# Kernel optimization log

Measured on AMD Instinct MI355X. Metric: run time of the kernel, lower is better.

## Reference

```python
import jax, jax.numpy as jnp
import numpy as np

R = 3            # window radius -> (2R+1)^2 = 49 neighbors
N = 128          # grid side, n
K = 131          # 3 + 64 + 64 channels
C = 21           # num_classes
B = 2            # batch
W = (2 * R + 1) ** 2


def setup_inputs() -> dict:
    key = jax.random.key(0)
    k1, k2, k3, k4 = jax.random.split(key, 4)
    return {
        "intergrated": jax.random.normal(k1, (B, K, N, N), jnp.float32),
        "x2": jax.random.normal(k2, (B, C, N * N), jnp.float32),
        "sel_mask": jax.random.randint(k3, (B, N, N), 0, 2).astype(jnp.int32),
        "conv_parameter": jax.random.uniform(k4, (K,), jnp.float32),
    }


def _shifts(x, r):
    """Gather (2r+1)^2 shifted copies: x [..., n, n] -> [..., n, n, W].
    Entry w=(di,dj) holds x[i+di-r, j+dj-r] (zero-padded out of bounds)."""
    n = x.shape[-1]
    pad = [(0, 0)] * (x.ndim - 2) + [(r, r), (r, r)]
    xp = jnp.pad(x, pad)
    cols = [xp[..., di:di + n, dj:dj + n]
            for di in range(2 * r + 1) for dj in range(2 * r + 1)]
    return jnp.stack(cols, axis=-1)


def _rwn_single(feats, x2b, maskb, conv_parameter):
    """feats [K,n,n], x2b [C,n^2], maskb [n,n] int -> y [n^2, C]."""
    n = feats.shape[-1]
    m = maskb.astype(feats.dtype)            # sampled-pixel indicator
    xm = feats * m                            # sparse-sampled features [K,n,n]
    nbr = _shifts(xm, R)                      # [K,n,n,W] neighbor values
    valid = _shifts(jnp.ones((n, n), feats.dtype), R) > 0  # [n,n,W] in-bounds
    # per-channel windowed L1 distance, exp, per-pixel normalization (softmax
    # of +distance over the valid window, as in the original code)
    d = jnp.abs(xm[..., None] - nbr)          # [K,n,n,W]
    e = jnp.where(valid[None], jnp.exp(d), 0.0)
    a = e / e.sum(axis=-1, keepdims=True)     # rows sum to 1 per channel
    # W = sum_k conv_parameter[k] * a_k, rows only for selected pixels
    A = jnp.einsum('k,kijw->ijw', conv_parameter, a) * m[..., None]  # [n,n,W]
    # y[q,c] = sum_p W[p,q] * x2[p,c]  (W^T @ x2^T, per original col/row swap)
    feat = x2b.reshape(C, n, n)
    msg = A[None] * feat[..., None]           # [C,n,n,W]
    ypad = jnp.zeros((C, n + 2 * R, n + 2 * R), feats.dtype)
    w = 0
    for di in range(2 * R + 1):
        for dj in range(2 * R + 1):
            ypad = ypad.at[:, di:di + n, dj:dj + n].add(msg[..., w])
            w += 1
    y = ypad[:, R:R + n, R:R + n].reshape(C, n * n)
    return y.T                                 # [n^2, C]


def reference(intergrated, x2, sel_mask, conv_parameter):
    f = lambda fe, xb, mb: _rwn_single(fe, xb, mb, conv_parameter)
    return jax.vmap(f)(intergrated, x2, sel_mask)  # [B, n^2, C]
```

## Files before the change

### kernel.cpp

```cpp
#include <hip/hip_runtime.h>
#include <hip/hip_fp16.h>

#define R_ 3
#define D_ 7
#define W_ 49
#define N_ 128
#define K_ 131
#define C_ 21
#define B_ 2
#define NN (N_ * N_)
#define TI_ 8
#define TJ_ 16
#define PROWS (TI_ + 2 * R_)
#define PCOLS (TJ_ + 2 * R_)
#define PSTR 24
#define NELEM (PROWS * PCOLS)
#define LDSP (PROWS * PSTR + 8)
#define KC 8
#define KCHUNK ((K_ + KC - 1) / KC)
#define HCELLS (PROWS * PCOLS)
#define NSLOT 28

typedef __fp16 h2 __attribute__((ext_vector_type(2)));

static __device__ __forceinline__ unsigned h2u(h2 x) { return __builtin_bit_cast(unsigned, x); }
static __device__ __forceinline__ h2 u2h(unsigned x) { return __builtin_bit_cast(h2, x); }

#if defined(__has_builtin)
#if __has_builtin(__builtin_amdgcn_fdot2)
#define FDOT2(a, b, c) __builtin_amdgcn_fdot2((a), (b), (c), false)
#endif
#endif
#ifndef FDOT2
#define FDOT2(a, b, c) ((c) + (float)(a)[0] * (float)(b)[0] + (float)(a)[1] * (float)(b)[1])
#endif

__global__ __launch_bounds__(256) void rwn_affinity_s(
    const float* __restrict__ feats,
    const int*   __restrict__ mask,
    const float* __restrict__ cp,
    unsigned* __restrict__ Asl)
{
    __shared__ unsigned patchw[LDSP];

    const int tile = blockIdx.x;
    const int kc   = blockIdx.y;
    const int b    = blockIdx.z;
    const int tr = tile >> 3, tc = tile & 7;
    const int ti0 = tr * TI_, tj0 = tc * TJ_;

    const int tid = threadIdx.x;
    const int pix = tid >> 1;
    const int h   = tid & 1;
    const int ti = pix >> 4;
    const int tj = pix & 15;
    const int gi = ti0 + ti, gj = tj0 + tj;

    const float LOG2E = 1.4426950408889634f;
    int   soff[2];
    float swt[2];
    float ozw[2];
    int   slds[2];
    #pragma unroll
    for (int r = 0; r < 2; ++r) {
        int e = tid + r * 256;
        bool act = (e < NELEM);
        int pr = e / PCOLS, pc = e - pr * PCOLS;
        int mi = ti0 + pr - R_, mj = tj0 + pc - R_;
        bool inb = act && mi >= 0 && mi < N_ && mj >= 0 && mj < N_;
        int cmi = mi < 0 ? 0 : (mi > N_ - 1 ? N_ - 1 : mi);
        int cmj = mj < 0 ? 0 : (mj > N_ - 1 ? N_ - 1 : mj);
        soff[r] = cmi * N_ + cmj;
        swt[r]  = inb ? ((float)mask[b * NN + soff[r]] * LOG2E) : 0.f;
        ozw[r]  = inb ? 1.f : 0.f;
        slds[r] = act ? (pr * PSTR + pc) : (PROWS * PSTR + 4);
    }

    const h2 ph2 = h ? (h2){(__fp16)1.f, (__fp16)0.f}
                     : (h2){(__fp16)1.f, (__fp16)1.f};
    const h2 one2 = (h2){(__fp16)1.f, (__fp16)1.f};
    const int cbase = (ti + R_) * PSTR + (tj + R_);
    const int bh = ti * PSTR + tj + 4 * h;

    h2 Aacc[14];
    #pragma unroll
    for (int i = 0; i < 14; ++i) Aacc[i] = (h2){(__fp16)0.f, (__fp16)0.f};

    const int k0 = kc * KCHUNK;
    const int k1 = (k0 + KCHUNK < K_) ? (k0 + KCHUNK) : K_;
    const float* fb = feats + (size_t)b * K_ * NN;

    for (int e = tid; e < LDSP; e += 256) patchw[e] = 0u;

    const float* fk0 = fb + (size_t)k0 * NN;
    float pre0 = fk0[soff[0]] * swt[0];
    float pre1 = fk0[soff[1]] * swt[1];

    __syncthreads();

    for (int k = k0; k < k1; ++k) {
        patchw[slds[0]] = h2u(__builtin_amdgcn_cvt_pkrtz(ozw[0] * exp2f(pre0),
                                                         ozw[0] * exp2f(-pre0)));
        patchw[slds[1]] = h2u(__builtin_amdgcn_cvt_pkrtz(ozw[1] * exp2f(pre1),
                                                         ozw[1] * exp2f(-pre1)));
        float n0 = 0.f, n1 = 0.f;
        if (k + 1 < k1) {
            const float* fn = fb + (size_t)(k + 1) * NN;
            n0 = fn[soff[0]] * swt[0];
            n1 = fn[soff[1]] * swt[1];
        }
        __syncthreads();

        const unsigned cw = patchw[cbase];
        const h2 cE2 = u2h(__builtin_amdgcn_perm(cw, cw, 0x01000100u));
        const h2 cI2 = u2h(__builtin_amdgcn_perm(cw, cw, 0x03020302u));

        h2 ex[14];
        float dsum = 0.f;
        #pragma unroll
        for (int u = 0; u < D_; ++u) {
            const int rb = bh + u * PSTR;
            const unsigned w0 = patchw[rb];
            const unsigned w1 = patchw[rb + 1];
            const unsigned w2 = patchw[rb + 2];
            const unsigned w3 = patchw[rb + 3];
            const h2 E01 = u2h(__builtin_amdgcn_perm(w1, w0, 0x05040100u));
            const h2 I01 = u2h(__builtin_amdgcn_perm(w1, w0, 0x07060302u));
            const h2 E23 = u2h(__builtin_amdgcn_perm(w3, w2, 0x05040100u));
            const h2 I23 = u2h(__builtin_amdgcn_perm(w3, w2, 0x07060302u));
            h2 t01 = __builtin_elementwise_max(cE2 * I01, E01 * cI2);
            h2 t23 = __builtin_elementwise_max(cE2 * I23, E23 * cI2);
            t23 = t23 * ph2;
            dsum = FDOT2(t01, one2, dsum);
            dsum = FDOT2(t23, one2, dsum);
            ex[u * 2]     = t01;
            ex[u * 2 + 1] = t23;
        }
        const float denom = dsum + __shfl_xor(dsum, 1, 64);
        const float scale = cp[k] * __frcp_rn(denom);
        const h2 s2 = __builtin_amdgcn_cvt_pkrtz(scale, scale);
        #pragma unroll
        for (int m = 0; m < 14; ++m) Aacc[m] = ex[m] * s2 + Aacc[m];
        __syncthreads();

        pre0 = n0; pre1 = n1;
    }

    const int mk = mask[b * NN + gi * N_ + gj];
    const h2 z2 = (h2){(__fp16)0.f, (__fp16)0.f};
    const int pixg = gi * N_ + gj;
    unsigned* ab = Asl + ((size_t)(kc * B_ + b) * NSLOT) * NN + pixg;
    #pragma unroll
    for (int u = 0; u < D_; ++u) {
        #pragma unroll
        for (int m = 0; m < 2; ++m) {
            const h2 tv = mk ? Aacc[u * 2 + m] : z2;
            ab[(size_t)(u * 4 + 2 * h + m) * NN] = h2u(tv);
        }
    }
}

__global__ __launch_bounds__(512) void rwn_gather_s(
    const unsigned* __restrict__ Asl,
    const float* __restrict__ x2,
    float* __restrict__ out)
{
    __shared__ float x2h[C_ * HCELLS];

    const int tile = blockIdx.x;
    const int b    = blockIdx.y;
    const int tr = tile >> 3, tc = tile & 7;
    const int gi0 = tr * TI_, gj0 = tc * TJ_;

    const int tid = threadIdx.x;

    const float* xb = x2 + (size_t)b * C_ * NN;
    for (int e = tid; e < C_ * HCELLS; e += 512) {
        const int c = e / HCELLS, cell = e - c * HCELLS;
        const int pr = cell / PCOLS, pc = cell - pr * PCOLS;
        const int mi = gi0 + pr - R_, mj = gj0 + pc - R_;
        const bool inb = (mi >= 0 && mi < N_ && mj >= 0 && mj < N_);
        const int cmi = mi < 0 ? 0 : (mi > N_ - 1 ? N_ - 1 : mi);
        const int cmj = mj < 0 ? 0 : (mj > N_ - 1 ? N_ - 1 : mj);
        x2h[e] = inb ? xb[c * NN + cmi * N_ + cmj] : 0.f;
    }
    __syncthreads();

    const int h = tid & 3;
    const int q = tid >> 2;
    const int qi = q >> 4, qj = q & 15;
    const int gi = gi0 + qi, gj = gj0 + qj;

    float av[13];
    int   cells[13];
    #pragma unroll
    for (int idx = 0; idx < 13; ++idx) {
        int w = h + 4 * idx;
        const float valid0 = (w < W_) ? 1.f : 0.f;
        if (w >= W_) w = 0;
        const int u = w / D_, vv = w - u * D_;
        const int s = vv >> 1, ln = vv & 1;
        const int pi = gi + R_ - u, pj = gj + R_ - vv;
        const int cmi = pi < 0 ? 0 : (pi > N_ - 1 ? N_ - 1 : pi);
        const int cmj = pj < 0 ? 0 : (pj > N_ - 1 ? N_ - 1 : pj);
        const float valid = (pi >= 0 && pi < N_ && pj >= 0 && pj < N_)
                          ? valid0 : 0.f;
        const int p = cmi * N_ + cmj;
        const size_t wordoff = (size_t)(u * 4 + s) * NN + p;
        float alo = 0.f, ahi = 0.f;
        #pragma unroll
        for (int kc = 0; kc < KC; ++kc) {
            const h2 pr2 = u2h(Asl[((size_t)(kc * B_ + b) * NSLOT) * NN + wordoff]);
            alo += (float)pr2[0];
            ahi += (float)pr2[1];
        }
        av[idx]    = valid * (ln ? ahi : alo);
        cells[idx] = (qi + 2 * R_ - u) * PCOLS + (qj + 2 * R_ - vv);
    }

    float acc[C_];
    #pragma unroll
    for (int c = 0; c < C_; ++c) acc[c] = 0.f;
    #pragma unroll
    for (int idx = 0; idx < 13; ++idx) {
        const float a = av[idx];
        const float* xc = x2h + cells[idx];
        #pragma unroll
        for (int c = 0; c < C_; ++c)
            acc[c] += a * xc[c * HCELLS];
    }

    #pragma unroll
    for (int c = 0; c < C_; ++c) {
        acc[c] += __shfl_xor(acc[c], 1, 64);
        acc[c] += __shfl_xor(acc[c], 2, 64);
    }

    __syncthreads();
    if (h == 0) {
        float* os = x2h + q * C_;
        #pragma unroll
        for (int c = 0; c < C_; ++c) os[c] = acc[c];
    }
    __syncthreads();
    for (int e = tid; e < TI_ * TJ_ * C_; e += 512) {
        const int qq = e / C_, cc = e - qq * C_;
        const int gq = (gi0 + (qq >> 4)) * N_ + gj0 + (qq & 15);
        out[((size_t)b * NN + gq) * C_ + cc] = x2h[e];
    }
}

__global__ __launch_bounds__(256) void rwn_affinity_at(
    const float* __restrict__ feats, const int* __restrict__ mask,
    const float* __restrict__ cp, float* __restrict__ Aout)
{
    __shared__ unsigned patchw[LDSP];
    const int tile = blockIdx.x, kc = blockIdx.y, b = blockIdx.z;
    const int tr = tile >> 3, tc = tile & 7;
    const int ti0 = tr * TI_, tj0 = tc * TJ_;
    const int tid = threadIdx.x;
    const int pix = tid >> 1, h = tid & 1;
    const int ti = pix >> 4, tj = pix & 15;
    const int gi = ti0 + ti, gj = tj0 + tj;
    const float LOG2E = 1.4426950408889634f;
    int soff[2]; float swt[2]; float ozw[2]; int slds[2];
    #pragma unroll
    for (int r = 0; r < 2; ++r) {
        int e = tid + r * 256;
        bool act = (e < NELEM);
        int pr = e / PCOLS, pc = e - pr * PCOLS;
        int mi = ti0 + pr - R_, mj = tj0 + pc - R_;
        bool inb = act && mi >= 0 && mi < N_ && mj >= 0 && mj < N_;
        int cmi = mi < 0 ? 0 : (mi > N_ - 1 ? N_ - 1 : mi);
        int cmj = mj < 0 ? 0 : (mj > N_ - 1 ? N_ - 1 : mj);
        soff[r] = cmi * N_ + cmj;
        swt[r]  = inb ? ((float)mask[b * NN + soff[r]] * LOG2E) : 0.f;
        ozw[r]  = inb ? 1.f : 0.f;
        slds[r] = act ? (pr * PSTR + pc) : (PROWS * PSTR + 4);
    }
    const h2 ph2 = h ? (h2){(__fp16)1.f, (__fp16)0.f}
                     : (h2){(__fp16)1.f, (__fp16)1.f};
    const h2 one2 = (h2){(__fp16)1.f, (__fp16)1.f};
    const int cbase = (ti + R_) * PSTR + (tj + R_);
    const int bh = ti * PSTR + tj + 4 * h;
    h2 Aacc[14];
    #pragma unroll
    for (int i = 0; i < 14; ++i) Aacc[i] = (h2){(__fp16)0.f, (__fp16)0.f};
    const int k0 = kc * KCHUNK;
    const int k1 = (k0 + KCHUNK < K_) ? (k0 + KCHUNK) : K_;
    const float* fb = feats + (size_t)b * K_ * NN;
    for (int e = tid; e < LDSP; e += 256) patchw[e] = 0u;
    const float* fk0 = fb + (size_t)k0 * NN;
    float pre0 = fk0[soff[0]] * swt[0];
    float pre1 = fk0[soff[1]] * swt[1];
    __syncthreads();
    for (int k = k0; k < k1; ++k) {
        patchw[slds[0]] = h2u(__builtin_amdgcn_cvt_pkrtz(ozw[0] * exp2f(pre0),
                                                         ozw[0] * exp2f(-pre0)));
        patchw[slds[1]] = h2u(__builtin_amdgcn_cvt_pkrtz(ozw[1] * exp2f(pre1),
                                                         ozw[1] * exp2f(-pre1)));
        float n0 = 0.f, n1 = 0.f;
        if (k + 1 < k1) {
            const float* fn = fb + (size_t)(k + 1) * NN;
            n0 = fn[soff[0]] * swt[0];
            n1 = fn[soff[1]] * swt[1];
        }
        __syncthreads();
        const unsigned cw = patchw[cbase];
        const h2 cE2 = u2h(__builtin_amdgcn_perm(cw, cw, 0x01000100u));
        const h2 cI2 = u2h(__builtin_amdgcn_perm(cw, cw, 0x03020302u));
        h2 ex[14];
        float dsum = 0.f;
        #pragma unroll
        for (int u = 0; u < D_; ++u) {
            const int rb = bh + u * PSTR;
            const unsigned w0 = patchw[rb];
            const unsigned w1 = patchw[rb + 1];
            const unsigned w2 = patchw[rb + 2];
            const unsigned w3 = patchw[rb + 3];
            const h2 E01 = u2h(__builtin_amdgcn_perm(w1, w0, 0x05040100u));
            const h2 I01 = u2h(__builtin_amdgcn_perm(w1, w0, 0x07060302u));
            const h2 E23 = u2h(__builtin_amdgcn_perm(w3, w2, 0x05040100u));
            const h2 I23 = u2h(__builtin_amdgcn_perm(w3, w2, 0x07060302u));
            h2 t01 = __builtin_elementwise_max(cE2 * I01, E01 * cI2);
            h2 t23 = __builtin_elementwise_max(cE2 * I23, E23 * cI2);
            t23 = t23 * ph2;
            dsum = FDOT2(t01, one2, dsum);
            dsum = FDOT2(t23, one2, dsum);
            ex[u * 2]     = t01;
            ex[u * 2 + 1] = t23;
        }
        const float denom = dsum + __shfl_xor(dsum, 1, 64);
        const float scale = cp[k] * __frcp_rn(denom);
        const h2 s2 = __builtin_amdgcn_cvt_pkrtz(scale, scale);
        #pragma unroll
        for (int m = 0; m < 14; ++m) Aacc[m] = ex[m] * s2 + Aacc[m];
        __syncthreads();
        pre0 = n0; pre1 = n1;
    }
    if (mask[b * NN + gi * N_ + gj] != 0) {
        const int pixg = gi * N_ + gj;
        float* ab = Aout + (size_t)b * W_ * NN + pixg;
        #pragma unroll
        for (int u = 0; u < D_; ++u) {
            #pragma unroll
            for (int m = 0; m < 2; ++m) {
                const h2 tv = Aacc[u * 2 + m];
                const int wbase = u * D_ + 4 * h + 2 * m;
                atomicAdd(ab + (size_t)wbase * NN, (float)tv[0]);
                if (h == 0 || m < 1)
                    atomicAdd(ab + (size_t)(wbase + 1) * NN, (float)tv[1]);
            }
        }
    }
}

__global__ __launch_bounds__(512) void rwn_gather_at(
    const float* __restrict__ Aarr, const float* __restrict__ x2,
    float* __restrict__ out)
{
    __shared__ float x2h[C_ * HCELLS];
    const int tile = blockIdx.x, b = blockIdx.y;
    const int tr = tile >> 3, tc = tile & 7;
    const int gi0 = tr * TI_, gj0 = tc * TJ_;
    const int tid = threadIdx.x;
    const float* xb = x2 + (size_t)b * C_ * NN;
    for (int e = tid; e < C_ * HCELLS; e += 512) {
        const int c = e / HCELLS, cell = e - c * HCELLS;
        const int pr = cell / PCOLS, pc = cell - pr * PCOLS;
        const int mi = gi0 + pr - R_, mj = gj0 + pc - R_;
        const bool inb = (mi >= 0 && mi < N_ && mj >= 0 && mj < N_);
        const int cmi = mi < 0 ? 0 : (mi > N_ - 1 ? N_ - 1 : mi);
        const int cmj = mj < 0 ? 0 : (mj > N_ - 1 ? N_ - 1 : mj);
        x2h[e] = inb ? xb[c * NN + cmi * N_ + cmj] : 0.f;
    }
    __syncthreads();
    const int h = tid & 3;
    const int q = tid >> 2;
    const int qi = q >> 4, qj = q & 15;
    const int gi = gi0 + qi, gj = gj0 + qj;
    const float* Ab = Aarr + (size_t)b * W_ * NN;
    float av[13];
    int   cells[13];
    #pragma unroll
    for (int idx = 0; idx < 13; ++idx) {
        int w = h + 4 * idx;
        const float valid = (w < W_) ? 1.f : 0.f;
        if (w >= W_) w = W_ - 1;
        const int u = w / D_, v = w - u * D_;
        const int pi = gi + R_ - u, pj = gj + R_ - v;
        const int cmi = pi < 0 ? 0 : (pi > N_ - 1 ? N_ - 1 : pi);
        const int cmj = pj < 0 ? 0 : (pj > N_ - 1 ? N_ - 1 : pj);
        av[idx]    = valid * Ab[(size_t)w * NN + cmi * N_ + cmj];
        cells[idx] = (qi + 2 * R_ - u) * PCOLS + (qj + 2 * R_ - v);
    }
    float acc[C_];
    #pragma unroll
    for (int c = 0; c < C_; ++c) acc[c] = 0.f;
    #pragma unroll
    for (int idx = 0; idx < 13; ++idx) {
        const float a = av[idx];
        const float* xc = x2h + cells[idx];
        #pragma unroll
        for (int c = 0; c < C_; ++c)
            acc[c] += a * xc[c * HCELLS];
    }
    #pragma unroll
    for (int c = 0; c < C_; ++c) {
        acc[c] += __shfl_xor(acc[c], 1, 64);
        acc[c] += __shfl_xor(acc[c], 2, 64);
    }
    __syncthreads();
    if (h == 0) {
        float* os = x2h + q * C_;
        #pragma unroll
        for (int c = 0; c < C_; ++c) os[c] = acc[c];
    }
    __syncthreads();
    for (int e = tid; e < TI_ * TJ_ * C_; e += 512) {
        const int qq = e / C_, cc = e - qq * C_;
        const int gq = (gi0 + (qq >> 4)) * N_ + gj0 + (qq & 15);
        out[((size_t)b * NN + gq) * C_ + cc] = x2h[e];
    }
}

extern "C" void kernel_launch(void* const* d_in, const int* in_sizes, int n_in,
                              void* d_out, int out_size, void* d_ws, size_t ws_size,
                              hipStream_t stream) {
    const float* feats = (const float*)d_in[0];
    const float* x2    = (const float*)d_in[1];
    const int*   mask  = (const int*)d_in[2];
    const float* cp    = (const float*)d_in[3];
    float* out = (float*)d_out;

    const size_t need = (size_t)KC * B_ * NSLOT * NN * sizeof(unsigned);

    if (ws_size >= need) {
        unsigned* Asl = (unsigned*)d_ws;
        dim3 gridA(128, KC, B_);
        rwn_affinity_s<<<gridA, 256, 0, stream>>>(feats, mask, cp, Asl);
        dim3 gridG(128, B_);
        rwn_gather_s<<<gridG, 512, 0, stream>>>(Asl, x2, out);
    } else {
        float* Aarr = (float*)d_ws;
        const size_t Abytes = (size_t)B_ * W_ * NN * sizeof(float);
        (void)hipMemsetAsync(Aarr, 0, Abytes, stream);
        dim3 gridA(128, KC, B_);
        rwn_affinity_at<<<gridA, 256, 0, stream>>>(feats, mask, cp, Aarr);
        dim3 gridG(128, B_);
        rwn_gather_at<<<gridG, 512, 0, stream>>>(Aarr, x2, out);
    }
}
```

Before: 138.3 us.

## Process two channels per iteration with packed half2 lanes in affinity kernel

```diff
diff --git a/kernel.cpp b/kernel.cpp
--- a/kernel.cpp
+++ b/kernel.cpp
@@ -16,24 +16,16 @@
 #define PSTR 24
 #define NELEM (PROWS * PCOLS)
 #define LDSP (PROWS * PSTR + 8)
-#define KC 8
-#define KCHUNK ((K_ + KC - 1) / KC)
+#define KC 6
+#define KCHUNK 22
 #define HCELLS (PROWS * PCOLS)
 #define NSLOT 28
 
 typedef __fp16 h2 __attribute__((ext_vector_type(2)));
+typedef __fp16 h4 __attribute__((ext_vector_type(4)));
 
 static __device__ __forceinline__ unsigned h2u(h2 x) { return __builtin_bit_cast(unsigned, x); }
 static __device__ __forceinline__ h2 u2h(unsigned x) { return __builtin_bit_cast(h2, x); }
-
-#if defined(__has_builtin)
-#if __has_builtin(__builtin_amdgcn_fdot2)
-#define FDOT2(a, b, c) __builtin_amdgcn_fdot2((a), (b), (c), false)
-#endif
-#endif
-#ifndef FDOT2
-#define FDOT2(a, b, c) ((c) + (float)(a)[0] * (float)(b)[0] + (float)(a)[1] * (float)(b)[1])
-#endif
 
 __global__ __launch_bounds__(256) void rwn_affinity_s(
     const float* __restrict__ feats,
@@ -41,7 +33,7 @@
     const float* __restrict__ cp,
     unsigned* __restrict__ Asl)
 {
-    __shared__ unsigned patchw[LDSP];
+    __shared__ h4 patch4[LDSP];
 
     const int tile = blockIdx.x;
     const int kc   = blockIdx.y;
@@ -76,86 +68,124 @@
         slds[r] = act ? (pr * PSTR + pc) : (PROWS * PSTR + 4);
     }
 
-    const h2 ph2 = h ? (h2){(__fp16)1.f, (__fp16)0.f}
+    const h2 ph2 = h ? (h2){(__fp16)0.f, (__fp16)0.f}
                      : (h2){(__fp16)1.f, (__fp16)1.f};
-    const h2 one2 = (h2){(__fp16)1.f, (__fp16)1.f};
     const int cbase = (ti + R_) * PSTR + (tj + R_);
     const int bh = ti * PSTR + tj + 4 * h;
 
-    h2 Aacc[14];
-    #pragma unroll
-    for (int i = 0; i < 14; ++i) Aacc[i] = (h2){(__fp16)0.f, (__fp16)0.f};
-
-    const int k0 = kc * KCHUNK;
-    const int k1 = (k0 + KCHUNK < K_) ? (k0 + KCHUNK) : K_;
+    h2 Aacc[28];
+    #pragma unroll
+    for (int i = 0; i < 28; ++i) Aacc[i] = (h2){(__fp16)0.f, (__fp16)0.f};
+
+    const int k0 = kc * 22;
+    const int k1 = (kc < 5) ? (k0 + 22) : K_;
     const float* fb = feats + (size_t)b * K_ * NN;
 
-    for (int e = tid; e < LDSP; e += 256) patchw[e] = 0u;
-
-    const float* fk0 = fb + (size_t)k0 * NN;
-    float pre0 = fk0[soff[0]] * swt[0];
-    float pre1 = fk0[soff[1]] * swt[1];
-
-    __syncthreads();
-
-    for (int k = k0; k < k1; ++k) {
-        patchw[slds[0]] = h2u(__builtin_amdgcn_cvt_pkrtz(ozw[0] * exp2f(pre0),
-                                                         ozw[0] * exp2f(-pre0)));
-        patchw[slds[1]] = h2u(__builtin_amdgcn_cvt_pkrtz(ozw[1] * exp2f(pre1),
-                                                         ozw[1] * exp2f(-pre1)));
-        float n0 = 0.f, n1 = 0.f;
-        if (k + 1 < k1) {
-            const float* fn = fb + (size_t)(k + 1) * NN;
-            n0 = fn[soff[0]] * swt[0];
-            n1 = fn[soff[1]] * swt[1];
-        }
+    {
+        h4 z4 = {};
+        for (int e = tid; e < LDSP; e += 256) patch4[e] = z4;
+    }
+
+    float a0, a1, b0, b1;
+    {
+        const float* fA = fb + (size_t)k0 * NN;
+        const float* fB = fb + (size_t)(k0 + 1) * NN;
+        a0 = fA[soff[0]] * swt[0];
+        a1 = fA[soff[1]] * swt[1];
+        b0 = fB[soff[0]] * swt[0];
+        b1 = fB[soff[1]] * swt[1];
+    }
+
+    __syncthreads();
+
+    const int npair = (k1 - k0 + 1) >> 1;
+    for (int p = 0; p < npair; ++p) {
+        const int kA = k0 + 2 * p;
+        const bool hasB = (kA + 1) < k1;
+
+        {
+            h2 E0 = __builtin_amdgcn_cvt_pkrtz(ozw[0] * exp2f(a0), ozw[0] * exp2f(b0));
+            h2 I0 = __builtin_amdgcn_cvt_pkrtz(ozw[0] * exp2f(-a0), ozw[0] * exp2f(-b0));
+            h2 E1 = __builtin_amdgcn_cvt_pkrtz(ozw[1] * exp2f(a1), ozw[1] * exp2f(b1));
+            h2 I1 = __builtin_amdgcn_cvt_pkrtz(ozw[1] * exp2f(-a1), ozw[1] * exp2f(-b1));
+            patch4[slds[0]] = __builtin_shufflevector(E0, I0, 0, 1, 2, 3);
+            patch4[slds[1]] = __builtin_shufflevector(E1, I1, 0, 1, 2, 3);
+        }
+
+        {
+            const int nA = kA + 2;
+            if (nA < k1) {
+                const float* f = fb + (size_t)nA * NN;
+                a0 = f[soff[0]] * swt[0];
+                a1 = f[soff[1]] * swt[1];
+            }
+            if (nA + 1 < k1) {
+                const float* f = fb + (size_t)(nA + 1) * NN;
+                b0 = f[soff[0]] * swt[0];
+                b1 = f[soff[1]] * swt[1];
+            } else { b0 = 0.f; b1 = 0.f; }
+        }
+
         __syncthreads();
 
-        const unsigned cw = patchw[cbase];
-        const h2 cE2 = u2h(__builtin_amdgcn_perm(cw, cw, 0x01000100u));
-        const h2 cI2 = u2h(__builtin_amdgcn_perm(cw, cw, 0x03020302u));
-
-        h2 ex[14];
-        float dsum = 0.f;
+        const h4 cc = patch4[cbase];
+        const h2 cE = __builtin_shufflevector(cc, cc, 0, 1);
+        const h2 cI = __builtin_shufflevector(cc, cc, 2, 3);
+        h2 ex[28];
+        float dsA = 0.f, dsB = 0.f;
         #pragma unroll
         for (int u = 0; u < D_; ++u) {
             const int rb = bh + u * PSTR;
-            const unsigned w0 = patchw[rb];
-            const unsigned w1 = patchw[rb + 1];
-            const unsigned w2 = patchw[rb + 2];
-            const unsigned w3 = patchw[rb + 3];
-            const h2 E01 = u2h(__builtin_amdgcn_perm(w1, w0, 0x05040100u));
-            const h2 I01 = u2h(__builtin_amdgcn_perm(w1, w0, 0x07060302u));
-            const h2 E23 = u2h(__builtin_amdgcn_perm(w3, w2, 0x05040100u));
-            const h2 I23 = u2h(__builtin_amdgcn_perm(w3, w2, 0x07060302u));
-            h2 t01 = __builtin_elementwise_max(cE2 * I01, E01 * cI2);
-            h2 t23 = __builtin_elementwise_max(cE2 * I23, E23 * cI2);
-            t23 = t23 * ph2;
-            dsum = FDOT2(t01, one2, dsum);
-            dsum = FDOT2(t23, one2, dsum);
-            ex[u * 2]     = t01;
-            ex[u * 2 + 1] = t23;
-        }
-        const float denom = dsum + __shfl_xor(dsum, 1, 64);
-        const float scale = cp[k] * __frcp_rn(denom);
-        const h2 s2 = __builtin_amdgcn_cvt_pkrtz(scale, scale);
-        #pragma unroll
-        for (int m = 0; m < 14; ++m) Aacc[m] = ex[m] * s2 + Aacc[m];
+            const h4 n0 = patch4[rb];
+            const h4 n1 = patch4[rb + 1];
+            const h4 n2 = patch4[rb + 2];
+            const h4 n3 = patch4[rb + 3];
+            h2 t0 = __builtin_elementwise_max(
+                cE * __builtin_shufflevector(n0, n0, 2, 3),
+                __builtin_shufflevector(n0, n0, 0, 1) * cI);
+            h2 t1 = __builtin_elementwise_max(
+                cE * __builtin_shufflevector(n1, n1, 2, 3),
+                __builtin_shufflevector(n1, n1, 0, 1) * cI);
+            h2 t2 = __builtin_elementwise_max(
+                cE * __builtin_shufflevector(n2, n2, 2, 3),
+                __builtin_shufflevector(n2, n2, 0, 1) * cI);
+            h2 t3 = __builtin_elementwise_max(
+                cE * __builtin_shufflevector(n3, n3, 2, 3),
+                __builtin_shufflevector(n3, n3, 0, 1) * cI);
+            t3 = t3 * ph2;
+            const h2 part = (t0 + t1) + (t2 + t3);
+            dsA += (float)part[0];
+            dsB += (float)part[1];
+            ex[u * 4 + 0] = t0;
+            ex[u * 4 + 1] = t1;
+            ex[u * 4 + 2] = t2;
+            ex[u * 4 + 3] = t3;
+        }
+        const float dA = dsA + __shfl_xor(dsA, 1, 64);
+        const float dB = dsB + __shfl_xor(dsB, 1, 64);
+        const float sA = cp[kA] * __frcp_rn(dA);
+        const float sB = (hasB ? cp[kA + 1] : 0.f) * __frcp_rn(dB);
+        const h2 s2 = __builtin_amdgcn_cvt_pkrtz(sA, sB);
+        #pragma unroll
+        for (int m = 0; m < 28; ++m) Aacc[m] = ex[m] * s2 + Aacc[m];
+
         __syncthreads();
-
-        pre0 = n0; pre1 = n1;
     }
 
     const int mk = mask[b * NN + gi * N_ + gj];
-    const h2 z2 = (h2){(__fp16)0.f, (__fp16)0.f};
+    const float fm = mk ? 1.f : 0.f;
     const int pixg = gi * N_ + gj;
     unsigned* ab = Asl + ((size_t)(kc * B_ + b) * NSLOT) * NN + pixg;
     #pragma unroll
     for (int u = 0; u < D_; ++u) {
         #pragma unroll
         for (int m = 0; m < 2; ++m) {
-            const h2 tv = mk ? Aacc[u * 2 + m] : z2;
-            ab[(size_t)(u * 4 + 2 * h + m) * NN] = h2u(tv);
+            const h2 pa = Aacc[u * 4 + 2 * m];
+            const h2 pb = Aacc[u * 4 + 2 * m + 1];
+            const float vA = fm * ((float)pa[0] + (float)pa[1]);
+            const float vB = fm * ((float)pb[0] + (float)pb[1]);
+            ab[(size_t)(u * 4 + 2 * h + m) * NN] =
+                h2u(__builtin_amdgcn_cvt_pkrtz(vA, vB));
         }
     }
 }
@@ -280,7 +310,6 @@
     }
     const h2 ph2 = h ? (h2){(__fp16)1.f, (__fp16)0.f}
                      : (h2){(__fp16)1.f, (__fp16)1.f};
-    const h2 one2 = (h2){(__fp16)1.f, (__fp16)1.f};
     const int cbase = (ti + R_) * PSTR + (tj + R_);
     const int bh = ti * PSTR + tj + 4 * h;
     h2 Aacc[14];
@@ -325,8 +354,8 @@
             h2 t01 = __builtin_elementwise_max(cE2 * I01, E01 * cI2);
             h2 t23 = __builtin_elementwise_max(cE2 * I23, E23 * cI2);
             t23 = t23 * ph2;
-            dsum = FDOT2(t01, one2, dsum);
-            dsum = FDOT2(t23, one2, dsum);
+            dsum += (float)t01[0] + (float)t01[1];
+            dsum += (float)t23[0] + (float)t23[1];
             ex[u * 2]     = t01;
             ex[u * 2 + 1] = t23;
         }
```

After: 130.1 us. -5.9%, faster.
